# Performance work log

Hardware: AMD Instinct MI355X
Metric: run time of the kernel (lower is better)

Reference implementation:

```python
import jax, jax.numpy as jnp
import numpy as np

N, DIN, D, H, L, S, E = 3072, 64, 128, 4, 2, 4, 49152
NEG = -2.0**32 + 1.0


def _layernorm(x, g, b, eps=1e-5):
    m = jnp.mean(x, axis=-1, keepdims=True)
    v = jnp.var(x, axis=-1, keepdims=True)
    return (x - m) * jax.lax.rsqrt(v + eps) * g + b


def setup_inputs() -> dict:
    key = jax.random.key(0)
    ks = jax.random.split(key, 24)
    w = lambda k, shp: (0.02 * jax.random.normal(k, shp)).astype(jnp.float32)
    inp = {
        "x": jax.random.normal(ks[0], (N, DIN), dtype=jnp.float32),
        "edge_index": jax.random.randint(ks[1], (2, E), 0, N, dtype=jnp.int64) if jax.config.jax_enable_x64 else jax.random.randint(ks[1], (2, E), 0, N).astype(jnp.int32),
        "shortest_path_len": jax.random.randint(ks[2], (N, N), 0, 11).astype(jnp.int32),
        "edge_feat": jax.random.normal(ks[3], (N, N, S), dtype=jnp.float32),
        # input projection
        "node_W": w(ks[4], (DIN, D)), "node_b": jnp.zeros((D,), jnp.float32),
        # centrality / spatial / edge encodings
        "deg_emb": w(ks[5], (N, D)),
        "sp_emb": w(ks[6], (11, 1)),
        "edge_W": w(ks[7], (S, S)), "edge_b": jnp.zeros((S,), jnp.float32),
        # per-layer stacked attention params
        "ln1_g": jnp.ones((L, D), jnp.float32), "ln1_b": jnp.zeros((L, D), jnp.float32),
        "Wq": w(ks[8], (L, H, D, D)), "bq": jnp.zeros((L, H, D), jnp.float32),
        "Wk": w(ks[9], (L, H, D, D)), "bk": jnp.zeros((L, H, D), jnp.float32),
        "Wv": w(ks[10], (L, H, D, D)), "bv": jnp.zeros((L, H, D), jnp.float32),
        "Wo": w(ks[11], (L, H * D, D)), "bo": jnp.zeros((L, D), jnp.float32),
        "ln2_g": jnp.ones((L, D), jnp.float32), "ln2_b": jnp.zeros((L, D), jnp.float32),
        "ff_W": w(ks[12], (L, D, D)), "ff_b": jnp.zeros((L, D), jnp.float32),
        # output projection
        "out_W": w(ks[13], (D, D)), "out_b": jnp.zeros((D,), jnp.float32),
    }
    return inp


def reference(x, edge_index, shortest_path_len, edge_feat,
              node_W, node_b, deg_emb, sp_emb, edge_W, edge_b,
              ln1_g, ln1_b, Wq, bq, Wk, bk, Wv, bv, Wo, bo,
              ln2_g, ln2_b, ff_W, ff_b, out_W, out_b):
    # padding mask from raw features
    mask_idx = (jnp.sum(x, axis=1) != 0).astype(x.dtype)            # [N]
    mask = mask_idx[:, None] * mask_idx[None, :]                    # [N,N]

    h = x @ node_W + node_b                                         # [N,D]
    # centrality: degree of edge destinations
    deg = jax.ops.segment_sum(jnp.ones((edge_index.shape[1],), jnp.int32),
                              edge_index[1], num_segments=N)        # [N]
    h = h + deg_emb[deg]

    spatial = sp_emb[shortest_path_len][..., 0]                     # [N,N]
    edge_m = (edge_feat @ edge_W + edge_b).mean(axis=-1)            # [N,N]
    bias = spatial + edge_m
    scale = 1.0 / jnp.sqrt(jnp.asarray(D, x.dtype))

    for l in range(L):
        x_ln = _layernorm(h, ln1_g[l], ln1_b[l])                    # [N,D]
        q = jnp.einsum('nd,hdk->hnk', x_ln, Wq[l]) + bq[l][:, None, :]
        k = jnp.einsum('nd,hdk->hnk', x_ln, Wk[l]) + bk[l][:, None, :]
        v = jnp.einsum('nd,hdk->hnk', x_ln, Wv[l]) + bv[l][:, None, :]
        a = jnp.einsum('hnk,hmk->hnm', q, k) * scale + bias[None]   # [H,N,N]
        a = jnp.where(mask[None] == 0, NEG, a)
        s = jax.nn.softmax(a, axis=-1)
        s = jnp.where(mask[None] == 0, 0.0, s)
        o = jnp.einsum('hnm,hmd->hnd', s, v)                        # [H,N,D]
        cat = jnp.transpose(o, (1, 0, 2)).reshape(N, H * D)         # [N,H*D]
        x_out = cat @ Wo[l] + bo[l] + h
        h = _layernorm(x_out, ln2_g[l], ln2_b[l]) @ ff_W[l] + ff_b[l] + x_out

    return h @ out_W + out_b
```

## Files before the change

kernel.cpp:

```cpp
#include <hip/hip_runtime.h>
#include <math.h>

static constexpr int N   = 3072;
static constexpr int DIN = 64;
static constexpr int D   = 128;
static constexpr int H   = 4;
static constexpr int E   = 49152;
#define NEGV  (-4294967295.0f)
#define SCALE (0.08838834764831845f)

typedef unsigned short u16;
typedef __attribute__((ext_vector_type(8))) short short8;
typedef __attribute__((ext_vector_type(4))) float f32x4;
typedef __attribute__((ext_vector_type(4))) unsigned short u16x4;

__device__ __forceinline__ u16 f2bf(float f){
  unsigned int u = __float_as_uint(f);
  u += 0x7fff + ((u >> 16) & 1);
  return (u16)(u >> 16);
}
__device__ __forceinline__ float bf2f(u16 u){
  return __uint_as_float(((unsigned int)u) << 16);
}

__global__ void k_zero_deg(int* __restrict__ deg){
  int i = blockIdx.x*blockDim.x + threadIdx.x;
  if(i < N) deg[i] = 0;
}

__global__ void k_deg(const int* __restrict__ ei, int* __restrict__ deg){
  int e = blockIdx.x*blockDim.x + threadIdx.x;
  if(e < E) atomicAdd(&deg[ei[E + e]], 1);
}

__global__ void k_h0(const float* __restrict__ x, const float* __restrict__ nodeW,
                     const float* __restrict__ nodeb, const float* __restrict__ degemb,
                     const int* __restrict__ deg, const float* __restrict__ g1,
                     const float* __restrict__ b1, float* __restrict__ mask,
                     float* __restrict__ h, float* __restrict__ xln){
  const int i = blockIdx.x, t = threadIdx.x;
  float xv = x[i*DIN + t];
  float s = xv;
  #pragma unroll
  for(int o=32;o;o>>=1) s += __shfl_xor(s, o);
  if(t == 0) mask[i] = (s != 0.0f) ? 1.0f : 0.0f;
  __shared__ float xr[DIN];
  xr[t] = xv;
  __syncthreads();
  int dg = deg[i]; dg = dg > N-1 ? N-1 : dg;
  float a0 = nodeb[t]      + degemb[dg*D + t];
  float a1 = nodeb[t + 64] + degemb[dg*D + t + 64];
  #pragma unroll
  for(int u=0; u<DIN; ++u){
    float xu = xr[u];
    a0 = fmaf(xu, nodeW[u*D + t],      a0);
    a1 = fmaf(xu, nodeW[u*D + t + 64], a1);
  }
  h[i*D + t]      = a0;
  h[i*D + t + 64] = a1;
  float s2 = a0 + a1, sq = a0*a0 + a1*a1;
  #pragma unroll
  for(int o=32;o;o>>=1){ s2 += __shfl_xor(s2, o); sq += __shfl_xor(sq, o); }
  float mean = s2*(1.0f/128.0f);
  float var  = sq*(1.0f/128.0f) - mean*mean;
  float inv  = rsqrtf(var + 1e-5f);
  xln[i*D + t]      = (a0 - mean)*inv*g1[t]      + b1[t];
  xln[i*D + t + 64] = (a1 - mean)*inv*g1[t + 64] + b1[t + 64];
}

__global__ void k_bias(const int* __restrict__ spl, const float* __restrict__ ef,
                       const float* __restrict__ spe, const float* __restrict__ eW,
                       const float* __restrict__ eb, const float* __restrict__ mask,
                       u16* __restrict__ biasm){
  int idx = blockIdx.x*blockDim.x + threadIdx.x;
  int i = idx / N, j = idx % N;
  float wm0 = (eW[0] + eW[1] + eW[2] + eW[3])  * 0.25f;
  float wm1 = (eW[4] + eW[5] + eW[6] + eW[7])  * 0.25f;
  float wm2 = (eW[8] + eW[9] + eW[10]+ eW[11]) * 0.25f;
  float wm3 = (eW[12]+ eW[13]+ eW[14]+ eW[15]) * 0.25f;
  float bm  = (eb[0] + eb[1] + eb[2] + eb[3])  * 0.25f;
  float4 e4 = reinterpret_cast<const float4*>(ef)[idx];
  float em = fmaf(e4.x, wm0, fmaf(e4.y, wm1, fmaf(e4.z, wm2, fmaf(e4.w, wm3, bm))));
  float b = spe[spl[idx]] + em;
  float mk = mask[i]*mask[j];
  biasm[idx] = f2bf((mk != 0.0f) ? b : NEGV);
}

__global__ __launch_bounds__(256) void k_wt_all(const float* __restrict__ Wq, const float* __restrict__ Wk,
    const float* __restrict__ Wv, const float* __restrict__ ffW, const float* __restrict__ outW,
    u16* __restrict__ wt_qkv, u16* __restrict__ wt_ff, u16* __restrict__ wt_out){
  __shared__ float t[32][33];
  const int z = blockIdx.y;
  const float* src; u16* dst;
  if(z < 24){
    int l = z/12, r = z%12;
    const float* W = (r>>2)==0 ? Wq : (r>>2)==1 ? Wk : Wv;
    src = W + (size_t)(l*4 + (r&3))*16384;
    dst = wt_qkv + (size_t)z*16384;
  } else if(z < 26){
    src = ffW + (size_t)(z-24)*16384; dst = wt_ff + (size_t)(z-24)*16384;
  } else { src = outW; dst = wt_out; }
  const int ki = blockIdx.x & 3, ni = blockIdx.x >> 2;
  const int tid = threadIdx.x;
  #pragma unroll
  for(int i=0;i<4;i++){
    int idx = tid + i*256, r = idx>>5, c = idx&31;
    t[r][c] = src[(size_t)(ki*32+r)*128 + ni*32 + c];
  }
  __syncthreads();
  #pragma unroll
  for(int i=0;i<4;i++){
    int idx = tid + i*256, r = idx>>5, c = idx&31;
    dst[(size_t)(ni*32+r)*128 + ki*32 + c] = f2bf(t[c][r]);
  }
}

__global__ __launch_bounds__(256) void k_wt_wo(const float* __restrict__ Wo, u16* __restrict__ wt_wo){
  __shared__ float t[32][33];
  const int l = blockIdx.y;
  const float* src = Wo + (size_t)l*65536;
  u16* dst = wt_wo + (size_t)l*65536;
  const int ki = blockIdx.x & 15, ni = blockIdx.x >> 4;
  const int tid = threadIdx.x;
  #pragma unroll
  for(int i=0;i<4;i++){
    int idx = tid + i*256, r = idx>>5, c = idx&31;
    t[r][c] = src[(size_t)(ki*32+r)*128 + ni*32 + c];
  }
  __syncthreads();
  #pragma unroll
  for(int i=0;i<4;i++){
    int idx = tid + i*256, r = idx>>5, c = idx&31;
    dst[(size_t)(ni*32+r)*512 + ki*32 + c] = f2bf(t[c][r]);
  }
}

template<int MODE>
__device__ __forceinline__ void mgemm_body(const float* __restrict__ A, const u16* __restrict__ Bt,
                                           const float* __restrict__ bias, void* __restrict__ Cv){
  __shared__ u16 As[64*128];
  __shared__ u16 Bs[128*128];
  const int tid = threadIdx.x, w = tid>>6, lane = tid&63;
  const int g4 = lane>>4, l16 = lane&15;
  const int m0 = blockIdx.x*64;
  const int srow = tid>>4, sch = tid&15;
  f32x4 acc[8];
  #pragma unroll
  for(int nt=0;nt<8;++nt) acc[nt] = (f32x4){0.f,0.f,0.f,0.f};
  #pragma unroll
  for(int it=0;it<4;++it){
    int row = it*16 + srow;
    const float4* ap = reinterpret_cast<const float4*>(A + (size_t)(m0+row)*128 + sch*8);
    float4 x0 = ap[0], x1 = ap[1];
    u16x4 p0, p1;
    p0.x=f2bf(x0.x); p0.y=f2bf(x0.y); p0.z=f2bf(x0.z); p0.w=f2bf(x0.w);
    p1.x=f2bf(x1.x); p1.y=f2bf(x1.y); p1.z=f2bf(x1.z); p1.w=f2bf(x1.w);
    u16* dst = &As[row*128 + ((sch ^ (row&15))*8)];
    *reinterpret_cast<u16x4*>(dst)     = p0;
    *reinterpret_cast<u16x4*>(dst + 4) = p1;
  }
  #pragma unroll
  for(int it=0;it<8;++it){
    int row = it*16 + srow;
    short8 b = *reinterpret_cast<const short8*>(Bt + (size_t)row*128 + sch*8);
    *reinterpret_cast<short8*>(&Bs[row*128 + ((sch ^ (row&15))*8)]) = b;
  }
  __syncthreads();
  __builtin_amdgcn_s_setprio(1);
  #pragma unroll
  for(int c=0;c<4;++c){
    short8 af = *reinterpret_cast<const short8*>(&As[(w*16+l16)*128 + (((c*4+g4) ^ l16)*8)]);
    #pragma unroll
    for(int nt=0;nt<8;++nt){
      short8 bf = *reinterpret_cast<const short8*>(&Bs[(nt*16+l16)*128 + (((c*4+g4) ^ l16)*8)]);
      acc[nt] = __builtin_amdgcn_mfma_f32_16x16x32_bf16(af, bf, acc[nt], 0, 0, 0);
    }
  }
  __builtin_amdgcn_s_setprio(0);
  const int mrow = m0 + w*16 + g4*4;
  if(MODE == 2){
    __syncthreads();
    u16* T = Bs;
    #pragma unroll
    for(int nt=0;nt<8;++nt){
      const int col = nt*16 + l16;
      float bi = bias[col];
      u16x4 t;
      t.x = f2bf(acc[nt][0] + bi); t.y = f2bf(acc[nt][1] + bi);
      t.z = f2bf(acc[nt][2] + bi); t.w = f2bf(acc[nt][3] + bi);
      *reinterpret_cast<u16x4*>(&T[col*68 + (w*16 + g4*4)]) = t;
    }
    __syncthreads();
    #pragma unroll
    for(int i=0;i<4;++i){
      int slot = tid + i*256;
      int col = slot >> 3, q = slot & 7;
      short8 v = *reinterpret_cast<const short8*>(&T[col*68 + q*8]);
      *reinterpret_cast<short8*>((u16*)Cv + (size_t)col*N + m0 + q*8) = v;
    }
  } else {
    #pragma unroll
    for(int nt=0;nt<8;++nt){
      const int col = nt*16 + l16;
      float bi = bias[col];
      #pragma unroll
      for(int rg=0;rg<4;++rg){
        float v = acc[nt][rg] + bi;
        if(MODE == 1) ((u16*)Cv)[(size_t)(mrow+rg)*128 + col] = f2bf(v);
        else          ((float*)Cv)[(size_t)(mrow+rg)*128 + col] = v;
      }
    }
  }
}

__global__ __launch_bounds__(256) void k_mqkv(const float* __restrict__ xln, const u16* __restrict__ wt_qkv,
    const float* __restrict__ bq, const float* __restrict__ bk, const float* __restrict__ bv,
    u16* __restrict__ q, u16* __restrict__ k, u16* __restrict__ vT, int l){
  const int z = blockIdx.y, which = z>>2, head = z&3;
  const u16* Bt = wt_qkv + (size_t)(l*12 + z)*16384;
  if(which == 0)      mgemm_body<1>(xln, Bt, bq + (l*H+head)*D, q  + (size_t)head*N*D);
  else if(which == 1) mgemm_body<1>(xln, Bt, bk + (l*H+head)*D, k  + (size_t)head*N*D);
  else                mgemm_body<2>(xln, Bt, bv + (l*H+head)*D, vT + (size_t)head*N*D);
}

__global__ __launch_bounds__(256) void k_mout(const float* __restrict__ h, const u16* __restrict__ wt_out,
    const float* __restrict__ outb, float* __restrict__ out){
  mgemm_body<0>(h, wt_out, outb, out);
}

template<int S>
__global__ __launch_bounds__(256) void k_mwo(const float* __restrict__ opart, const float* __restrict__ mpart,
    const float* __restrict__ lpart, const float* __restrict__ mask, const u16* __restrict__ wt,
    const float* __restrict__ bo, const float* __restrict__ hres,
    float* __restrict__ xout, float* __restrict__ xln,
    const float* __restrict__ g2, const float* __restrict__ b2){
  __shared__ u16 As[64*128];
  __shared__ u16 Bs[128*128];
  const int tid = threadIdx.x, w = tid>>6, lane = tid&63;
  const int g4 = lane>>4, l16 = lane&15;
  const int m0 = blockIdx.x*64;
  const int srow = tid>>4, sch = tid&15;
  f32x4 acc[8];
  #pragma unroll
  for(int nt=0;nt<8;++nt) acc[nt] = (f32x4){0.f,0.f,0.f,0.f};
  for(int k0 = 0; k0 < 512; k0 += 128){
    const int hh = k0 >> 7;
    __syncthreads();
    #pragma unroll
    for(int it=0;it<4;++it){
      int row = it*16 + srow;
      int grow = m0 + row;
      float w_[S]; float M = -INFINITY; float mv[S], lv[S];
      #pragma unroll
      for(int s=0;s<S;++s){
        mv[s] = mpart[(size_t)(s*H + hh)*N + grow];
        lv[s] = lpart[(size_t)(s*H + hh)*N + grow];
        M = fmaxf(M, mv[s]);
      }
      float denom = 0.f;
      #pragma unroll
      for(int s=0;s<S;++s){ w_[s] = __expf(mv[s] - M); denom = fmaf(lv[s], w_[s], denom); }
      float scale = mask[grow] / denom;
      const int d = sch*8;
      float4 v0 = make_float4(0,0,0,0), v1 = make_float4(0,0,0,0);
      #pragma unroll
      for(int s=0;s<S;++s){
        const float4* op = reinterpret_cast<const float4*>(
            opart + ((size_t)(s*H + hh)*N + grow)*D + d);
        float4 a = op[0], b = op[1];
        v0.x = fmaf(a.x, w_[s], v0.x); v0.y = fmaf(a.y, w_[s], v0.y);
        v0.z = fmaf(a.z, w_[s], v0.z); v0.w = fmaf(a.w, w_[s], v0.w);
        v1.x = fmaf(b.x, w_[s], v1.x); v1.y = fmaf(b.y, w_[s], v1.y);
        v1.z = fmaf(b.z, w_[s], v1.z); v1.w = fmaf(b.w, w_[s], v1.w);
      }
      u16x4 p0, p1;
      p0.x=f2bf(v0.x*scale); p0.y=f2bf(v0.y*scale); p0.z=f2bf(v0.z*scale); p0.w=f2bf(v0.w*scale);
      p1.x=f2bf(v1.x*scale); p1.y=f2bf(v1.y*scale); p1.z=f2bf(v1.z*scale); p1.w=f2bf(v1.w*scale);
      u16* dst = &As[row*128 + ((sch ^ (row&15))*8)];
      *reinterpret_cast<u16x4*>(dst)     = p0;
      *reinterpret_cast<u16x4*>(dst + 4) = p1;
    }
    #pragma unroll
    for(int it=0;it<8;++it){
      int row = it*16 + srow;
      short8 b = *reinterpret_cast<const short8*>(wt + (size_t)row*512 + k0 + sch*8);
      *reinterpret_cast<short8*>(&Bs[row*128 + ((sch ^ (row&15))*8)]) = b;
    }
    __syncthreads();
    __builtin_amdgcn_s_setprio(1);
    #pragma unroll
    for(int c=0;c<4;++c){
      short8 af = *reinterpret_cast<const short8*>(&As[(w*16+l16)*128 + (((c*4+g4) ^ l16)*8)]);
      #pragma unroll
      for(int nt=0;nt<8;++nt){
        short8 bf = *reinterpret_cast<const short8*>(&Bs[(nt*16+l16)*128 + (((c*4+g4) ^ l16)*8)]);
        acc[nt] = __builtin_amdgcn_mfma_f32_16x16x32_bf16(af, bf, acc[nt], 0, 0, 0);
      }
    }
    __builtin_amdgcn_s_setprio(0);
  }
  const int mrow = m0 + w*16 + g4*4;
  float s_[4] = {0,0,0,0}, q_[4] = {0,0,0,0};
  #pragma unroll
  for(int nt=0;nt<8;++nt){
    const int col = nt*16 + l16;
    float bi = bo[col];
    #pragma unroll
    for(int rg=0;rg<4;++rg){
      float v = acc[nt][rg] + bi + hres[(size_t)(mrow+rg)*128 + col];
      acc[nt][rg] = v;
      s_[rg] += v; q_[rg] = fmaf(v, v, q_[rg]);
    }
  }
  #pragma unroll
  for(int o=1;o<16;o<<=1){
    #pragma unroll
    for(int rg=0;rg<4;++rg){ s_[rg] += __shfl_xor(s_[rg], o); q_[rg] += __shfl_xor(q_[rg], o); }
  }
  float mean[4], inv[4];
  #pragma unroll
  for(int rg=0;rg<4;++rg){
    mean[rg] = s_[rg]*(1.0f/128.0f);
    float var = q_[rg]*(1.0f/128.0f) - mean[rg]*mean[rg];
    inv[rg] = rsqrtf(var + 1e-5f);
  }
  #pragma unroll
  for(int nt=0;nt<8;++nt){
    const int col = nt*16 + l16;
    float gg = g2[col], bb = b2[col];
    #pragma unroll
    for(int rg=0;rg<4;++rg){
      float v = acc[nt][rg];
      xout[(size_t)(mrow+rg)*128 + col] = v;
      xln [(size_t)(mrow+rg)*128 + col] = (v - mean[rg])*inv[rg]*gg + bb;
    }
  }
}

__global__ __launch_bounds__(256) void k_mff(const float* __restrict__ xlnin, const u16* __restrict__ wt,
    const float* __restrict__ ffb, const float* __restrict__ res, float* __restrict__ hout,
    float* __restrict__ xlnout, const float* __restrict__ g1n, const float* __restrict__ b1n,
    int write_ln){
  __shared__ u16 As[64*128];
  __shared__ u16 Bs[128*128];
  const int tid = threadIdx.x, w = tid>>6, lane = tid&63;
  const int g4 = lane>>4, l16 = lane&15;
  const int m0 = blockIdx.x*64;
  const int srow = tid>>4, sch = tid&15;
  f32x4 acc[8];
  #pragma unroll
  for(int nt=0;nt<8;++nt) acc[nt] = (f32x4){0.f,0.f,0.f,0.f};
  #pragma unroll
  for(int it=0;it<4;++it){
    int row = it*16 + srow;
    const float4* ap = reinterpret_cast<const float4*>(xlnin + (size_t)(m0+row)*128 + sch*8);
    float4 x0 = ap[0], x1 = ap[1];
    u16x4 p0, p1;
    p0.x=f2bf(x0.x); p0.y=f2bf(x0.y); p0.z=f2bf(x0.z); p0.w=f2bf(x0.w);
    p1.x=f2bf(x1.x); p1.y=f2bf(x1.y); p1.z=f2bf(x1.z); p1.w=f2bf(x1.w);
    u16* dst = &As[row*128 + ((sch ^ (row&15))*8)];
    *reinterpret_cast<u16x4*>(dst)     = p0;
    *reinterpret_cast<u16x4*>(dst + 4) = p1;
  }
  #pragma unroll
  for(int it=0;it<8;++it){
    int row = it*16 + srow;
    short8 b = *reinterpret_cast<const short8*>(wt + (size_t)row*128 + sch*8);
    *reinterpret_cast<short8*>(&Bs[row*128 + ((sch ^ (row&15))*8)]) = b;
  }
  __syncthreads();
  __builtin_amdgcn_s_setprio(1);
  #pragma unroll
  for(int c=0;c<4;++c){
    short8 af = *reinterpret_cast<const short8*>(&As[(w*16+l16)*128 + (((c*4+g4) ^ l16)*8)]);
    #pragma unroll
    for(int nt=0;nt<8;++nt){
      short8 bf = *reinterpret_cast<const short8*>(&Bs[(nt*16+l16)*128 + (((c*4+g4) ^ l16)*8)]);
      acc[nt] = __builtin_amdgcn_mfma_f32_16x16x32_bf16(af, bf, acc[nt], 0, 0, 0);
    }
  }
  __builtin_amdgcn_s_setprio(0);
  const int mrow = m0 + w*16 + g4*4;
  float s_[4] = {0,0,0,0}, q_[4] = {0,0,0,0};
  #pragma unroll
  for(int nt=0;nt<8;++nt){
    const int col = nt*16 + l16;
    float bi = ffb[col];
    #pragma unroll
    for(int rg=0;rg<4;++rg){
      float v = acc[nt][rg] + bi + res[(size_t)(mrow+rg)*128 + col];
      acc[nt][rg] = v;
      s_[rg] += v; q_[rg] = fmaf(v, v, q_[rg]);
    }
  }
  #pragma unroll
  for(int nt=0;nt<8;++nt){
    const int col = nt*16 + l16;
    #pragma unroll
    for(int rg=0;rg<4;++rg)
      hout[(size_t)(mrow+rg)*128 + col] = acc[nt][rg];
  }
  if(write_ln){
    #pragma unroll
    for(int o=1;o<16;o<<=1){
      #pragma unroll
      for(int rg=0;rg<4;++rg){ s_[rg] += __shfl_xor(s_[rg], o); q_[rg] += __shfl_xor(q_[rg], o); }
    }
    #pragma unroll
    for(int rg=0;rg<4;++rg){
      float mean = s_[rg]*(1.0f/128.0f);
      float var  = q_[rg]*(1.0f/128.0f) - mean*mean;
      float inv  = rsqrtf(var + 1e-5f);
      s_[rg] = mean; q_[rg] = inv;
    }
    #pragma unroll
    for(int nt=0;nt<8;++nt){
      const int col = nt*16 + l16;
      float gg = g1n[col], bb = b1n[col];
      #pragma unroll
      for(int rg=0;rg<4;++rg)
        xlnout[(size_t)(mrow+rg)*128 + col] = (acc[nt][rg] - s_[rg])*q_[rg]*gg + bb;
    }
  }
}

__global__ __launch_bounds__(256) void k_attn(const u16* __restrict__ q, const u16* __restrict__ k,
                     const u16* __restrict__ vT, const u16* __restrict__ biasm,
                     float* __restrict__ opart, float* __restrict__ mpart, float* __restrict__ lpart,
                     int kvlen){
  const int tid  = threadIdx.x;
  const int w    = tid >> 6;
  const int lane = tid & 63;
  const int g4 = lane >> 4, l16 = lane & 15;
  const int head = blockIdx.y, sp = blockIdx.z;
  const int r0 = blockIdx.x*128 + w*32;
  __shared__ u16 Ks[64*128];
  __shared__ u16 Vs[64*128];
  __shared__ u16 P[4][2][16][40];

  const u16* qbase = q + ((size_t)head*N + r0)*D;
  short8 qf0[4], qf1[4];
  #pragma unroll
  for(int c=0;c<4;c++){
    qf0[c] = *reinterpret_cast<const short8*>(qbase + l16*D + c*32 + g4*8);
    qf1[c] = *reinterpret_cast<const short8*>(qbase + (16+l16)*D + c*32 + g4*8);
  }

  f32x4 o0[8], o1[8];
  #pragma unroll
  for(int dt=0;dt<8;dt++){ o0[dt] = (f32x4){0.f,0.f,0.f,0.f}; o1[dt] = o0[dt]; }
  float m0v = -INFINITY, ls0 = 0.0f;
  float m1v = -INFINITY, ls1 = 0.0f;

  const u16* kh   = k  + (size_t)head*N*D;
  const u16* vTh  = vT + (size_t)head*D*N;
  const u16* brow0 = biasm + (size_t)(r0 + l16)*N;
  const u16* brow1 = biasm + (size_t)(r0 + 16 + l16)*N;
  const int kv0 = sp*kvlen;

  const int krow = tid >> 4, kch = tid & 15;
  const int vrow = tid >> 3, vch = tid & 7;

  for(int j0 = kv0; j0 < kv0 + kvlen; j0 += 64){
    short8 kreg[4], vreg[4];
    #pragma unroll
    for(int it=0; it<4; ++it)
      kreg[it] = *reinterpret_cast<const short8*>(kh + (size_t)(j0 + it*16 + krow)*D + kch*8);
    #pragma unroll
    for(int it=0; it<4; ++it)
      vreg[it] = *reinterpret_cast<const short8*>(vTh + (size_t)(it*32 + vrow)*N + j0 + vch*8);
    u16x4 bb0[4], bb1[4];
    #pragma unroll
    for(int z=0; z<4; ++z){
      bb0[z] = *reinterpret_cast<const u16x4*>(brow0 + j0 + z*16 + g4*4);
      bb1[z] = *reinterpret_cast<const u16x4*>(brow1 + j0 + z*16 + g4*4);
    }

    __syncthreads();
    #pragma unroll
    for(int it=0; it<4; ++it){
      int row = it*16 + krow;
      *reinterpret_cast<short8*>(&Ks[row*128 + ((kch ^ (row&15))*8)]) = kreg[it];
    }
    #pragma unroll
    for(int it=0; it<4; ++it){
      int d = it*32 + vrow;
      int row = d & 63, ch = ((d>>6)<<3) | vch;
      *reinterpret_cast<short8*>(&Vs[row*128 + ((ch ^ (row&15))*8)]) = vreg[it];
    }
    __syncthreads();

    #pragma unroll
    for(int ks=0; ks<2; ++ks){
      short8 kf[8];
      const int rowA = ks*32 + l16, rowB = rowA + 16;
      #pragma unroll
      for(int c=0;c<4;c++){
        kf[c]   = *reinterpret_cast<const short8*>(&Ks[rowA*128 + (((c*4+g4) ^ l16)*8)]);
        kf[4+c] = *reinterpret_cast<const short8*>(&Ks[rowB*128 + (((c*4+g4) ^ l16)*8)]);
      }
      f32x4 sA0 = (f32x4){0.f,0.f,0.f,0.f}, sB0 = sA0, sA1 = sA0, sB1 = sA0;
      __builtin_amdgcn_s_setprio(1);
      #pragma unroll
      for(int c=0;c<4;c++){
        sA0 = __builtin_amdgcn_mfma_f32_16x16x32_bf16(kf[c],   qf0[c], sA0, 0, 0, 0);
        sB0 = __builtin_amdgcn_mfma_f32_16x16x32_bf16(kf[4+c], qf0[c], sB0, 0, 0, 0);
        sA1 = __builtin_amdgcn_mfma_f32_16x16x32_bf16(kf[c],   qf1[c], sA1, 0, 0, 0);
        sB1 = __builtin_amdgcn_mfma_f32_16x16x32_bf16(kf[4+c], qf1[c], sB1, 0, 0, 0);
      }
      __builtin_amdgcn_s_setprio(0);
      {
        u16x4 bA = bb0[2*ks], bB = bb0[2*ks+1];
        sA0[0] = fmaf(sA0[0], SCALE, bf2f(bA.x)); sA0[1] = fmaf(sA0[1], SCALE, bf2f(bA.y));
        sA0[2] = fmaf(sA0[2], SCALE, bf2f(bA.z)); sA0[3] = fmaf(sA0[3], SCALE, bf2f(bA.w));
        sB0[0] = fmaf(sB0[0], SCALE, bf2f(bB.x)); sB0[1] = fmaf(sB0[1], SCALE, bf2f(bB.y));
        sB0[2] = fmaf(sB0[2], SCALE, bf2f(bB.z)); sB0[3] = fmaf(sB0[3], SCALE, bf2f(bB.w));
      }
      {
        u16x4 bA = bb1[2*ks], bB = bb1[2*ks+1];
        sA1[0] = fmaf(sA1[0], SCALE, bf2f(bA.x)); sA1[1] = fmaf(sA1[1], SCALE, bf2f(bA.y));
        sA1[2] = fmaf(sA1[2], SCALE, bf2f(bA.z)); sA1[3] = fmaf(sA1[3], SCALE, bf2f(bA.w));
        sB1[0] = fmaf(sB1[0], SCALE, bf2f(bB.x)); sB1[1] = fmaf(sB1[1], SCALE, bf2f(bB.y));
        sB1[2] = fmaf(sB1[2], SCALE, bf2f(bB.z)); sB1[3] = fmaf(sB1[3], SCALE, bf2f(bB.w));
      }
      float p0 = fmaxf(fmaxf(fmaxf(sA0[0],sA0[1]), fmaxf(sA0[2],sA0[3])),
                       fmaxf(fmaxf(sB0[0],sB0[1]), fmaxf(sB0[2],sB0[3])));
      float p1 = fmaxf(fmaxf(fmaxf(sA1[0],sA1[1]), fmaxf(sA1[2],sA1[3])),
                       fmaxf(fmaxf(sB1[0],sB1[1]), fmaxf(sB1[2],sB1[3])));
      p0 = fmaxf(p0, __shfl_xor(p0, 16)); p0 = fmaxf(p0, __shfl_xor(p0, 32));
      p1 = fmaxf(p1, __shfl_xor(p1, 16)); p1 = fmaxf(p1, __shfl_xor(p1, 32));
      float dm = fmaxf(p0 - m0v, p1 - m1v);
      if(!__all(dm <= 8.0f)){
        float mn0 = fmaxf(m0v, p0), mn1 = fmaxf(m1v, p1);
        float cr0 = __expf(m0v - mn0), cr1 = __expf(m1v - mn1);
        ls0 *= cr0; ls1 *= cr1;
        #pragma unroll
        for(int rg=0;rg<4;++rg){
          float c0 = __shfl(cr0, (lane & 48) | (g4*4 + rg));
          float c1 = __shfl(cr1, (lane & 48) | (g4*4 + rg));
          #pragma unroll
          for(int dt=0;dt<8;dt++){ o0[dt][rg] *= c0; o1[dt][rg] *= c1; }
        }
        m0v = mn0; m1v = mn1;
      }
      f32x4 pA0, pB0, pA1, pB1;
      #pragma unroll
      for(int rg=0;rg<4;rg++){
        pA0[rg] = __expf(sA0[rg] - m0v); pB0[rg] = __expf(sB0[rg] - m0v);
        pA1[rg] = __expf(sA1[rg] - m1v); pB1[rg] = __expf(sB1[rg] - m1v);
      }
      float ps0 = (pA0[0]+pA0[1]) + (pA0[2]+pA0[3]) + ((pB0[0]+pB0[1]) + (pB0[2]+pB0[3]));
      float ps1 = (pA1[0]+pA1[1]) + (pA1[2]+pA1[3]) + ((pB1[0]+pB1[1]) + (pB1[2]+pB1[3]));
      ps0 += __shfl_xor(ps0, 16); ps0 += __shfl_xor(ps0, 32);
      ps1 += __shfl_xor(ps1, 16); ps1 += __shfl_xor(ps1, 32);
      ls0 += ps0; ls1 += ps1;
      u16x4 wa, wb;
      wa.x = f2bf(pA0[0]); wa.y = f2bf(pA0[1]); wa.z = f2bf(pA0[2]); wa.w = f2bf(pA0[3]);
      wb.x = f2bf(pB0[0]); wb.y = f2bf(pB0[1]); wb.z = f2bf(pB0[2]); wb.w = f2bf(pB0[3]);
      *reinterpret_cast<u16x4*>(&P[w][0][l16][g4*4])      = wa;
      *reinterpret_cast<u16x4*>(&P[w][0][l16][16 + g4*4]) = wb;
      wa.x = f2bf(pA1[0]); wa.y = f2bf(pA1[1]); wa.z = f2bf(pA1[2]); wa.w = f2bf(pA1[3]);
      wb.x = f2bf(pB1[0]); wb.y = f2bf(pB1[1]); wb.z = f2bf(pB1[2]); wb.w = f2bf(pB1[3]);
      *reinterpret_cast<u16x4*>(&P[w][1][l16][g4*4])      = wa;
      *reinterpret_cast<u16x4*>(&P[w][1][l16][16 + g4*4]) = wb;
      short8 pf0 = *reinterpret_cast<const short8*>(&P[w][0][l16][g4*8]);
      short8 pf1 = *reinterpret_cast<const short8*>(&P[w][1][l16][g4*8]);
      __builtin_amdgcn_s_setprio(1);
      #pragma unroll
      for(int dt=0;dt<8;dt++){
        int d = dt*16 + l16;
        int row = d & 63;
        int ch  = ((dt>>2)<<3) | (ks<<2) | g4;
        short8 vf = *reinterpret_cast<const short8*>(&Vs[row*128 + ((ch ^ l16)*8)]);
        o0[dt] = __builtin_amdgcn_mfma_f32_16x16x32_bf16(pf0, vf, o0[dt], 0, 0, 0);
        o1[dt] = __builtin_amdgcn_mfma_f32_16x16x32_bf16(pf1, vf, o1[dt], 0, 0, 0);
      }
      __builtin_amdgcn_s_setprio(0);
    }
  }

  float* ob0 = opart + ((size_t)((sp*H + head)*N) + r0)*D;
  float* ob1 = ob0 + (size_t)16*D;
  #pragma unroll
  for(int dt=0;dt<8;dt++){
    #pragma unroll
    for(int rg=0;rg<4;rg++){
      ob0[(size_t)(g4*4+rg)*D + dt*16 + l16] = o0[dt][rg];
      ob1[(size_t)(g4*4+rg)*D + dt*16 + l16] = o1[dt][rg];
    }
  }
  if(g4 == 0){
    mpart[(size_t)(sp*H + head)*N + r0 + l16]      = m0v;
    lpart[(size_t)(sp*H + head)*N + r0 + l16]      = ls0;
    mpart[(size_t)(sp*H + head)*N + r0 + 16 + l16] = m1v;
    lpart[(size_t)(sp*H + head)*N + r0 + 16 + l16] = ls1;
  }
}

extern "C" void kernel_launch(void* const* d_in, const int* in_sizes, int n_in,
                              void* d_out, int out_size, void* d_ws, size_t ws_size,
                              hipStream_t stream){
  const float* x      = (const float*)d_in[0];
  const int*   ei     = (const int*)  d_in[1];
  const int*   spl    = (const int*)  d_in[2];
  const float* ef     = (const float*)d_in[3];
  const float* nodeW  = (const float*)d_in[4];
  const float* nodeb  = (const float*)d_in[5];
  const float* degemb = (const float*)d_in[6];
  const float* spe    = (const float*)d_in[7];
  const float* eW     = (const float*)d_in[8];
  const float* eb     = (const float*)d_in[9];
  const float* ln1g   = (const float*)d_in[10];
  const float* ln1b   = (const float*)d_in[11];
  const float* Wq     = (const float*)d_in[12];
  const float* bq     = (const float*)d_in[13];
  const float* Wk     = (const float*)d_in[14];
  const float* bk     = (const float*)d_in[15];
  const float* Wv     = (const float*)d_in[16];
  const float* bv     = (const float*)d_in[17];
  const float* Wo     = (const float*)d_in[18];
  const float* bo     = (const float*)d_in[19];
  const float* ln2g   = (const float*)d_in[20];
  const float* ln2b   = (const float*)d_in[21];
  const float* ffW    = (const float*)d_in[22];
  const float* ffb    = (const float*)d_in[23];
  const float* outW   = (const float*)d_in[24];
  const float* outb   = (const float*)d_in[25];

  constexpr size_t WT_ELEMS = 24*16384 + 2*16384 + 16384 + 2*65536;
  auto needed = [](int s)->size_t{
    size_t fl = 8192 + 3*(size_t)N*D;
    size_t bf = 3*(size_t)H*N*D + (size_t)N*N;
    size_t pf = (size_t)s*H*N*D + 2*(size_t)s*H*N;
    return fl*4 + bf*2 + pf*4 + WT_ELEMS*2;
  };
  int S = 2;
  if(needed(8) <= ws_size) S = 8;
  else if(needed(4) <= ws_size) S = 4;

  float* ws   = (float*)d_ws;
  int*   deg  = (int*)ws;
  float* mask = ws + 4096;
  float* h    = ws + 8192;
  float* xln  = h    + N*D;
  float* xout = xln  + N*D;
  u16*   qb   = (u16*)(xout + N*D);
  u16*   kb   = qb + (size_t)H*N*D;
  u16*   vTb  = kb + (size_t)H*N*D;
  u16*   biasm= vTb + (size_t)H*N*D;
  float* opart= (float*)(biasm + (size_t)N*N);
  float* mpart= opart + (size_t)S*H*N*D;
  float* lpart= mpart + (size_t)S*H*N;
  u16*   wt_qkv = (u16*)(lpart + (size_t)S*H*N);
  u16*   wt_ff  = wt_qkv + 24*16384;
  u16*   wt_out = wt_ff  + 2*16384;
  u16*   wt_wo  = wt_out + 16384;

  k_wt_all<<<dim3(16, 27), 256, 0, stream>>>(Wq, Wk, Wv, ffW, outW, wt_qkv, wt_ff, wt_out);
  k_wt_wo<<<dim3(64, 2), 256, 0, stream>>>(Wo, wt_wo);
  k_zero_deg<<<(N+255)/256, 256, 0, stream>>>(deg);
  k_deg<<<(E+255)/256, 256, 0, stream>>>(ei, deg);
  k_h0<<<N, 64, 0, stream>>>(x, nodeW, nodeb, degemb, deg, ln1g, ln1b, mask, h, xln);
  k_bias<<<(N*N)/256, 256, 0, stream>>>(spl, ef, spe, eW, eb, mask, biasm);

  for(int l = 0; l < 2; ++l){
    k_mqkv<<<dim3(N/64, 12), 256, 0, stream>>>(xln, wt_qkv, bq, bk, bv, qb, kb, vTb, l);
    k_attn<<<dim3(N/128, H, S), 256, 0, stream>>>(qb, kb, vTb, biasm, opart, mpart, lpart, N/S);
    if(S == 8)
      k_mwo<8><<<N/64, 256, 0, stream>>>(opart, mpart, lpart, mask, wt_wo + (size_t)l*65536,
                                         bo + l*D, h, xout, xln, ln2g + l*D, ln2b + l*D);
    else if(S == 4)
      k_mwo<4><<<N/64, 256, 0, stream>>>(opart, mpart, lpart, mask, wt_wo + (size_t)l*65536,
                                         bo + l*D, h, xout, xln, ln2g + l*D, ln2b + l*D);
    else
      k_mwo<2><<<N/64, 256, 0, stream>>>(opart, mpart, lpart, mask, wt_wo + (size_t)l*65536,
                                         bo + l*D, h, xout, xln, ln2g + l*D, ln2b + l*D);
    k_mff<<<N/64, 256, 0, stream>>>(xln, wt_ff + (size_t)l*16384, ffb + l*D, xout, h, xln,
                                    ln1g + (l==0 ? D : 0), ln1b + (l==0 ? D : 0), l==0 ? 1 : 0);
  }
  k_mout<<<N/64, 256, 0, stream>>>(h, wt_out, outb, (float*)d_out);
}
```

Measured before the change: 272.8 us.

## Store split-KV attention partials in bf16 and move bias loads into inner loop

```diff
diff --git a/kernel.cpp b/kernel.cpp
--- a/kernel.cpp
+++ b/kernel.cpp
@@ -229,7 +229,7 @@
 }
 
 template<int S>
-__global__ __launch_bounds__(256) void k_mwo(const float* __restrict__ opart, const float* __restrict__ mpart,
+__global__ __launch_bounds__(256) void k_mwo(const u16* __restrict__ opart, const float* __restrict__ mpart,
     const float* __restrict__ lpart, const float* __restrict__ mask, const u16* __restrict__ wt,
     const float* __restrict__ bo, const float* __restrict__ hres,
     float* __restrict__ xout, float* __restrict__ xln,
@@ -262,20 +262,17 @@
       for(int s=0;s<S;++s){ w_[s] = __expf(mv[s] - M); denom = fmaf(lv[s], w_[s], denom); }
       float scale = mask[grow] / denom;
       const int d = sch*8;
-      float4 v0 = make_float4(0,0,0,0), v1 = make_float4(0,0,0,0);
+      float v[8] = {0,0,0,0,0,0,0,0};
       #pragma unroll
       for(int s=0;s<S;++s){
-        const float4* op = reinterpret_cast<const float4*>(
+        short8 ov = *reinterpret_cast<const short8*>(
             opart + ((size_t)(s*H + hh)*N + grow)*D + d);
-        float4 a = op[0], b = op[1];
-        v0.x = fmaf(a.x, w_[s], v0.x); v0.y = fmaf(a.y, w_[s], v0.y);
-        v0.z = fmaf(a.z, w_[s], v0.z); v0.w = fmaf(a.w, w_[s], v0.w);
-        v1.x = fmaf(b.x, w_[s], v1.x); v1.y = fmaf(b.y, w_[s], v1.y);
-        v1.z = fmaf(b.z, w_[s], v1.z); v1.w = fmaf(b.w, w_[s], v1.w);
+        #pragma unroll
+        for(int j=0;j<8;++j) v[j] = fmaf(bf2f((u16)ov[j]), w_[s], v[j]);
       }
       u16x4 p0, p1;
-      p0.x=f2bf(v0.x*scale); p0.y=f2bf(v0.y*scale); p0.z=f2bf(v0.z*scale); p0.w=f2bf(v0.w*scale);
-      p1.x=f2bf(v1.x*scale); p1.y=f2bf(v1.y*scale); p1.z=f2bf(v1.z*scale); p1.w=f2bf(v1.w*scale);
+      p0.x=f2bf(v[0]*scale); p0.y=f2bf(v[1]*scale); p0.z=f2bf(v[2]*scale); p0.w=f2bf(v[3]*scale);
+      p1.x=f2bf(v[4]*scale); p1.y=f2bf(v[5]*scale); p1.z=f2bf(v[6]*scale); p1.w=f2bf(v[7]*scale);
       u16* dst = &As[row*128 + ((sch ^ (row&15))*8)];
       *reinterpret_cast<u16x4*>(dst)     = p0;
       *reinterpret_cast<u16x4*>(dst + 4) = p1;
@@ -424,9 +421,9 @@
   }
 }
 
-__global__ __launch_bounds__(256) void k_attn(const u16* __restrict__ q, const u16* __restrict__ k,
+__global__ __launch_bounds__(256, 3) void k_attn(const u16* __restrict__ q, const u16* __restrict__ k,
                      const u16* __restrict__ vT, const u16* __restrict__ biasm,
-                     float* __restrict__ opart, float* __restrict__ mpart, float* __restrict__ lpart,
+                     u16* __restrict__ opart, float* __restrict__ mpart, float* __restrict__ lpart,
                      int kvlen){
   const int tid  = threadIdx.x;
   const int w    = tid >> 6;
@@ -469,12 +466,6 @@
     #pragma unroll
     for(int it=0; it<4; ++it)
       vreg[it] = *reinterpret_cast<const short8*>(vTh + (size_t)(it*32 + vrow)*N + j0 + vch*8);
-    u16x4 bb0[4], bb1[4];
-    #pragma unroll
-    for(int z=0; z<4; ++z){
-      bb0[z] = *reinterpret_cast<const u16x4*>(brow0 + j0 + z*16 + g4*4);
-      bb1[z] = *reinterpret_cast<const u16x4*>(brow1 + j0 + z*16 + g4*4);
-    }
 
     __syncthreads();
     #pragma unroll
@@ -492,6 +483,10 @@
 
     #pragma unroll
     for(int ks=0; ks<2; ++ks){
+      u16x4 bA0 = *reinterpret_cast<const u16x4*>(brow0 + j0 + ks*32 + g4*4);
+      u16x4 bB0 = *reinterpret_cast<const u16x4*>(brow0 + j0 + ks*32 + 16 + g4*4);
+      u16x4 bA1 = *reinterpret_cast<const u16x4*>(brow1 + j0 + ks*32 + g4*4);
+      u16x4 bB1 = *reinterpret_cast<const u16x4*>(brow1 + j0 + ks*32 + 16 + g4*4);
       short8 kf[8];
       const int rowA = ks*32 + l16, rowB = rowA + 16;
       #pragma unroll
@@ -509,20 +504,14 @@
         sB1 = __builtin_amdgcn_mfma_f32_16x16x32_bf16(kf[4+c], qf1[c], sB1, 0, 0, 0);
       }
       __builtin_amdgcn_s_setprio(0);
-      {
-        u16x4 bA = bb0[2*ks], bB = bb0[2*ks+1];
-        sA0[0] = fmaf(sA0[0], SCALE, bf2f(bA.x)); sA0[1] = fmaf(sA0[1], SCALE, bf2f(bA.y));
-        sA0[2] = fmaf(sA0[2], SCALE, bf2f(bA.z)); sA0[3] = fmaf(sA0[3], SCALE, bf2f(bA.w));
-        sB0[0] = fmaf(sB0[0], SCALE, bf2f(bB.x)); sB0[1] = fmaf(sB0[1], SCALE, bf2f(bB.y));
-        sB0[2] = fmaf(sB0[2], SCALE, bf2f(bB.z)); sB0[3] = fmaf(sB0[3], SCALE, bf2f(bB.w));
-      }
-      {
-        u16x4 bA = bb1[2*ks], bB = bb1[2*ks+1];
-        sA1[0] = fmaf(sA1[0], SCALE, bf2f(bA.x)); sA1[1] = fmaf(sA1[1], SCALE, bf2f(bA.y));
-        sA1[2] = fmaf(sA1[2], SCALE, bf2f(bA.z)); sA1[3] = fmaf(sA1[3], SCALE, bf2f(bA.w));
-        sB1[0] = fmaf(sB1[0], SCALE, bf2f(bB.x)); sB1[1] = fmaf(sB1[1], SCALE, bf2f(bB.y));
-        sB1[2] = fmaf(sB1[2], SCALE, bf2f(bB.z)); sB1[3] = fmaf(sB1[3], SCALE, bf2f(bB.w));
-      }
+      sA0[0] = fmaf(sA0[0], SCALE, bf2f(bA0.x)); sA0[1] = fmaf(sA0[1], SCALE, bf2f(bA0.y));
+      sA0[2] = fmaf(sA0[2], SCALE, bf2f(bA0.z)); sA0[3] = fmaf(sA0[3], SCALE, bf2f(bA0.w));
+      sB0[0] = fmaf(sB0[0], SCALE, bf2f(bB0.x)); sB0[1] = fmaf(sB0[1], SCALE, bf2f(bB0.y));
+      sB0[2] = fmaf(sB0[2], SCALE, bf2f(bB0.z)); sB0[3] = fmaf(sB0[3], SCALE, bf2f(bB0.w));
+      sA1[0] = fmaf(sA1[0], SCALE, bf2f(bA1.x)); sA1[1] = fmaf(sA1[1], SCALE, bf2f(bA1.y));
+      sA1[2] = fmaf(sA1[2], SCALE, bf2f(bA1.z)); sA1[3] = fmaf(sA1[3], SCALE, bf2f(bA1.w));
+      sB1[0] = fmaf(sB1[0], SCALE, bf2f(bB1.x)); sB1[1] = fmaf(sB1[1], SCALE, bf2f(bB1.y));
+      sB1[2] = fmaf(sB1[2], SCALE, bf2f(bB1.z)); sB1[3] = fmaf(sB1[3], SCALE, bf2f(bB1.w));
       float p0 = fmaxf(fmaxf(fmaxf(sA0[0],sA0[1]), fmaxf(sA0[2],sA0[3])),
                        fmaxf(fmaxf(sB0[0],sB0[1]), fmaxf(sB0[2],sB0[3])));
       float p1 = fmaxf(fmaxf(fmaxf(sA1[0],sA1[1]), fmaxf(sA1[2],sA1[3])),
@@ -579,14 +568,14 @@
     }
   }
 
-  float* ob0 = opart + ((size_t)((sp*H + head)*N) + r0)*D;
-  float* ob1 = ob0 + (size_t)16*D;
+  u16* ob0 = opart + ((size_t)((sp*H + head)*N) + r0)*D;
+  u16* ob1 = ob0 + (size_t)16*D;
   #pragma unroll
   for(int dt=0;dt<8;dt++){
     #pragma unroll
     for(int rg=0;rg<4;rg++){
-      ob0[(size_t)(g4*4+rg)*D + dt*16 + l16] = o0[dt][rg];
-      ob1[(size_t)(g4*4+rg)*D + dt*16 + l16] = o1[dt][rg];
+      ob0[(size_t)(g4*4+rg)*D + dt*16 + l16] = f2bf(o0[dt][rg]);
+      ob1[(size_t)(g4*4+rg)*D + dt*16 + l16] = f2bf(o1[dt][rg]);
     }
   }
   if(g4 == 0){
@@ -630,8 +619,8 @@
   constexpr size_t WT_ELEMS = 24*16384 + 2*16384 + 16384 + 2*65536;
   auto needed = [](int s)->size_t{
     size_t fl = 8192 + 3*(size_t)N*D;
-    size_t bf = 3*(size_t)H*N*D + (size_t)N*N;
-    size_t pf = (size_t)s*H*N*D + 2*(size_t)s*H*N;
+    size_t bf = 3*(size_t)H*N*D + (size_t)N*N + (size_t)s*H*N*D;
+    size_t pf = 2*(size_t)s*H*N;
     return fl*4 + bf*2 + pf*4 + WT_ELEMS*2;
   };
   int S = 2;
@@ -648,8 +637,8 @@
   u16*   kb   = qb + (size_t)H*N*D;
   u16*   vTb  = kb + (size_t)H*N*D;
   u16*   biasm= vTb + (size_t)H*N*D;
-  float* opart= (float*)(biasm + (size_t)N*N);
-  float* mpart= opart + (size_t)S*H*N*D;
+  u16*   opart= biasm + (size_t)N*N;
+  float* mpart= (float*)(opart + (size_t)S*H*N*D);
   float* lpart= mpart + (size_t)S*H*N;
   u16*   wt_qkv = (u16*)(lpart + (size_t)S*H*N);
   u16*   wt_ff  = wt_qkv + 24*16384;
```

Result: faster. 246.6 us (-9.6%).
